# Kernel optimization log

Hardware: AMD Instinct MI355X
Metric: run time of the kernel (lower is better)

The kernel has to match this reference:

```python
import jax, jax.numpy as jnp
import numpy as np

def setup_inputs() -> dict:
    key = jax.random.key(0)
    S = jax.random.normal(key, (8192, 16384), dtype=jnp.float32)
    return {"S": S}

def reference(S):
    # L21 norm: sum over columns of the per-column L2 norm.
    # Single fused pass: per-column sum of squares -> sqrt -> sum.
    col_norms = jnp.sqrt(jnp.sum(S * S, axis=0))  # [n]
    return jnp.sum(col_norms)
```

## Files before the change

### kernel.cpp

```cpp
#include <hip/hip_runtime.h>


#define N_ROWS 8192
#define N_COLS 16384
#define CHUNKS 64
#define ROWS_PER_CHUNK (N_ROWS / CHUNKS)
#define THREADS 256
#define COLS_PER_BLOCK (THREADS * 4)

__global__ __launch_bounds__(THREADS) void l21_partial_kernel(
    const float* __restrict__ S, float* __restrict__ partial) {
    const int col4 = blockIdx.x * COLS_PER_BLOCK + threadIdx.x * 4;
    const int r0   = blockIdx.y * ROWS_PER_CHUNK;

    const float4* p = (const float4*)(S + (size_t)r0 * N_COLS + col4);
    float4 acc = make_float4(0.f, 0.f, 0.f, 0.f);
#pragma unroll 16
    for (int r = 0; r < ROWS_PER_CHUNK; ++r) {
        float4 v = p[(size_t)r * (N_COLS / 4)];
        acc.x += v.x * v.x;
        acc.y += v.y * v.y;
        acc.z += v.z * v.z;
        acc.w += v.w * v.w;
    }
    *(float4*)(partial + (size_t)blockIdx.y * N_COLS + col4) = acc;
}

__global__ __launch_bounds__(THREADS) void l21_finish_kernel(
    const float* __restrict__ partial, float* __restrict__ out) {
    const int col = blockIdx.x * THREADS + threadIdx.x;

    float s = 0.f;
#pragma unroll
    for (int c = 0; c < CHUNKS; ++c)
        s += partial[(size_t)c * N_COLS + col];
    float v = sqrtf(s);

#pragma unroll
    for (int off = 32; off > 0; off >>= 1)
        v += __shfl_down(v, off, 64);

    __shared__ float wsum[THREADS / 64];
    const int lane = threadIdx.x & 63;
    const int wave = threadIdx.x >> 6;
    if (lane == 0) wsum[wave] = v;
    __syncthreads();

    if (threadIdx.x == 0) {
        float t = 0.f;
#pragma unroll
        for (int w = 0; w < THREADS / 64; ++w) t += wsum[w];
        atomicAdd(out, t);
    }
}

extern "C" void kernel_launch(void* const* d_in, const int* in_sizes, int n_in,
                              void* d_out, int out_size, void* d_ws, size_t ws_size,
                              hipStream_t stream) {
    const float* S = (const float*)d_in[0];
    float* out     = (float*)d_out;
    float* partial = (float*)d_ws;

    hipMemsetAsync(out, 0, sizeof(float), stream);

    dim3 grid1(N_COLS / COLS_PER_BLOCK, CHUNKS);
    l21_partial_kernel<<<grid1, THREADS, 0, stream>>>(S, partial);

    dim3 grid2(N_COLS / THREADS);
    l21_finish_kernel<<<grid2, THREADS, 0, stream>>>(partial, out);
}
```

Baseline: 698.9 us.

## Restructure partial reduction so each block sweeps full rows in short chunks

The partial kernel now gives each block a 16-row chunk spanning every column, with each thread keeping 16 float4 accumulators, instead of a 2D grid of column tiles by 128-row chunks. The aim is more independent loads in flight per thread and fully contiguous row reads. In exchange there are 512 chunks instead of 64, so the partial buffer grows eightfold. The finish kernel, still only 64 blocks, must now serially sum 512 values per column with its unroll removed, which risks making that pass latency-bound. The larger buffer may also exceed the workspace.

New measurement: 694.1 us. About the same (-0.7%).

```diff
diff --git a/kernel.cpp b/kernel.cpp
--- a/kernel.cpp
+++ b/kernel.cpp
@@ -3,27 +3,36 @@
 
 #define N_ROWS 8192
 #define N_COLS 16384
-#define CHUNKS 64
-#define ROWS_PER_CHUNK (N_ROWS / CHUNKS)
 #define THREADS 256
-#define COLS_PER_BLOCK (THREADS * 4)
+#define ROWS_PER_CHUNK 16
+#define CHUNKS (N_ROWS / ROWS_PER_CHUNK)
+#define SEGS (N_COLS / (THREADS * 4))
 
 __global__ __launch_bounds__(THREADS) void l21_partial_kernel(
     const float* __restrict__ S, float* __restrict__ partial) {
-    const int col4 = blockIdx.x * COLS_PER_BLOCK + threadIdx.x * 4;
-    const int r0   = blockIdx.y * ROWS_PER_CHUNK;
+    const int chunk = blockIdx.x;
+    const size_t base = (size_t)chunk * ROWS_PER_CHUNK * N_COLS;
 
-    const float4* p = (const float4*)(S + (size_t)r0 * N_COLS + col4);
-    float4 acc = make_float4(0.f, 0.f, 0.f, 0.f);
-#pragma unroll 16
+    float4 acc[SEGS];
+#pragma unroll
+    for (int s = 0; s < SEGS; ++s) acc[s] = make_float4(0.f, 0.f, 0.f, 0.f);
+
+    const float4* p = (const float4*)(S + base) + threadIdx.x;
     for (int r = 0; r < ROWS_PER_CHUNK; ++r) {
-        float4 v = p[(size_t)r * (N_COLS / 4)];
-        acc.x += v.x * v.x;
-        acc.y += v.y * v.y;
-        acc.z += v.z * v.z;
-        acc.w += v.w * v.w;
+        const float4* row = p + (size_t)r * (N_COLS / 4);
+#pragma unroll
+        for (int s = 0; s < SEGS; ++s) {
+            float4 v = row[s * THREADS];
+            acc[s].x += v.x * v.x;
+            acc[s].y += v.y * v.y;
+            acc[s].z += v.z * v.z;
+            acc[s].w += v.w * v.w;
+        }
     }
-    *(float4*)(partial + (size_t)blockIdx.y * N_COLS + col4) = acc;
+
+    float4* q = (float4*)(partial + (size_t)chunk * N_COLS) + threadIdx.x;
+#pragma unroll
+    for (int s = 0; s < SEGS; ++s) q[s * THREADS] = acc[s];
 }
 
 __global__ __launch_bounds__(THREADS) void l21_finish_kernel(
@@ -31,7 +40,6 @@
     const int col = blockIdx.x * THREADS + threadIdx.x;
 
     float s = 0.f;
-#pragma unroll
     for (int c = 0; c < CHUNKS; ++c)
         s += partial[(size_t)c * N_COLS + col];
     float v = sqrtf(s);
@@ -63,9 +71,7 @@
 
     hipMemsetAsync(out, 0, sizeof(float), stream);
 
-    dim3 grid1(N_COLS / COLS_PER_BLOCK, CHUNKS);
-    l21_partial_kernel<<<grid1, THREADS, 0, stream>>>(S, partial);
+    l21_partial_kernel<<<dim3(CHUNKS), THREADS, 0, stream>>>(S, partial);
 
-    dim3 grid2(N_COLS / THREADS);
-    l21_finish_kernel<<<grid2, THREADS, 0, stream>>>(partial, out);
+    l21_finish_kernel<<<dim3(N_COLS / THREADS), THREADS, 0, stream>>>(partial, out);
 }
```
